# Performance work log

Hardware: AMD Instinct MI355X
Metric: run time of the kernel (lower is better)

Reference implementation:

```python
import jax, jax.numpy as jnp
import numpy as np

NUM_HEADS = 12
HEAD_DIM = 64
SCALE = HEAD_DIM ** -0.5


def setup_inputs() -> dict:
    key = jax.random.key(0)
    ks = jax.random.split(key, 5)
    B, N, C = 8, 1024, 768
    x = jax.random.normal(ks[0], (B, N, C), dtype=jnp.float32)
    qkv_w = jax.random.normal(ks[1], (3 * C, C), dtype=jnp.float32) * (C ** -0.5)
    qkv_b = jax.random.normal(ks[2], (3 * C,), dtype=jnp.float32) * 0.02
    proj_w = jax.random.normal(ks[3], (C, C), dtype=jnp.float32) * (C ** -0.5)
    proj_b = jax.random.normal(ks[4], (C,), dtype=jnp.float32) * 0.02
    return {"x": x, "qkv_w": qkv_w, "qkv_b": qkv_b, "proj_w": proj_w, "proj_b": proj_b}


def reference(x, qkv_w, qkv_b, proj_w, proj_b):
    B, N, C = x.shape
    H, D = NUM_HEADS, HEAD_DIM
    # qkv projection: (B,N,3C) -> (3,B,H,N,D)
    qkv = (x @ qkv_w.T + qkv_b).reshape(B, N, 3, H, D).transpose(2, 0, 3, 1, 4)
    q, k, v = qkv[0], qkv[1], qkv[2]
    q = q * SCALE
    # full N x N attention scores, softmax over keys
    attn = jax.nn.softmax(jnp.einsum("bhnd,bhmd->bhnm", q, k), axis=-1)
    # Libragrad: detach the softmax map before multiplying with V
    attn = jax.lax.stop_gradient(attn)
    out = jnp.einsum("bhnm,bhmd->bhnd", attn, v)  # (B,H,N,D)
    out = out.transpose(0, 2, 1, 3).reshape(B, N, C)
    return out @ proj_w.T + proj_b
```

## Files before the change

kernel.cpp:

```cpp
#include <hip/hip_runtime.h>

#define NH 12
#define HD 64
#define BB 8
#define SEQ 1024
#define CD 768

typedef __bf16 bf16x8 __attribute__((ext_vector_type(8)));
typedef float f32x4 __attribute__((ext_vector_type(4)));

__device__ __forceinline__ unsigned short f2bf(float f) {
    unsigned int u = __float_as_uint(f);
    u = (u + 0x7fffu + ((u >> 16) & 1u)) >> 16;
    return (unsigned short)u;
}

__device__ __forceinline__ void gld_lds16(const unsigned short* g, unsigned short* l) {
    __builtin_amdgcn_global_load_lds(
        (const __attribute__((address_space(1))) unsigned int*)g,
        (__attribute__((address_space(3))) unsigned int*)l, 16, 0, 0);
}

#define N4_X 1572864
#define N4_W1 442368
#define N4_W2 147456
__global__ void cast_all(const float* __restrict__ x, const float* __restrict__ w1,
                         const float* __restrict__ w2,
                         unsigned short* __restrict__ ox, unsigned short* __restrict__ ow1,
                         unsigned short* __restrict__ ow2) {
    int i = blockIdx.x * blockDim.x + threadIdx.x;
    const float4* src;
    ushort4* dst;
    if (i < N4_X) {
        src = (const float4*)x + i; dst = (ushort4*)ox + i;
    } else if (i < N4_X + N4_W1) {
        src = (const float4*)w1 + (i - N4_X); dst = (ushort4*)ow1 + (i - N4_X);
    } else if (i < N4_X + N4_W1 + N4_W2) {
        src = (const float4*)w2 + (i - N4_X - N4_W1); dst = (ushort4*)ow2 + (i - N4_X - N4_W1);
    } else return;
    float4 f = *src;
    ushort4 o;
    o.x = f2bf(f.x); o.y = f2bf(f.y); o.z = f2bf(f.z); o.w = f2bf(f.w);
    *dst = o;
}

template<int MODE>
__global__ __launch_bounds__(256)
void gemm_bt(const unsigned short* __restrict__ A, const unsigned short* __restrict__ W,
             const float* __restrict__ bias,
             unsigned short* __restrict__ qb, unsigned short* __restrict__ kb,
             unsigned short* __restrict__ vb, float* __restrict__ fout,
             int M, int N, int K) {
    __shared__ __attribute__((aligned(16))) unsigned short As[128 * 32];
    __shared__ __attribute__((aligned(16))) unsigned short Bs[128 * 32];

    const int t    = threadIdx.x;
    const int bn0  = blockIdx.x * 128;
    const int bm0  = blockIdx.y * 128;
    const int wave = t >> 6;
    const int lane = t & 63;
    const int wm   = (wave >> 1) * 64;
    const int wn   = (wave & 1) * 64;
    const int col  = lane & 15;
    const int quad = lane >> 4;

    const int srow = t >> 2;
    const int scol = (t & 3) * 8;

    f32x4 acc[4][4];
#pragma unroll
    for (int i = 0; i < 4; i++)
#pragma unroll
        for (int j = 0; j < 4; j++) acc[i][j] = (f32x4){0.f, 0.f, 0.f, 0.f};

    for (int k0 = 0; k0 < K; k0 += 32) {
        __syncthreads();
        gld_lds16(A + (size_t)(bm0 + srow) * K + k0 + scol,      As + srow * 32 + scol);
        gld_lds16(A + (size_t)(bm0 + 64 + srow) * K + k0 + scol, As + (64 + srow) * 32 + scol);
        gld_lds16(W + (size_t)(bn0 + srow) * K + k0 + scol,      Bs + srow * 32 + scol);
        gld_lds16(W + (size_t)(bn0 + 64 + srow) * K + k0 + scol, Bs + (64 + srow) * 32 + scol);
        __syncthreads();

        bf16x8 af[4], bf[4];
#pragma unroll
        for (int mi = 0; mi < 4; mi++)
            af[mi] = *(const bf16x8*)(As + (wm + mi * 16 + col) * 32 + quad * 8);
#pragma unroll
        for (int ni = 0; ni < 4; ni++)
            bf[ni] = *(const bf16x8*)(Bs + (wn + ni * 16 + col) * 32 + quad * 8);
#pragma unroll
        for (int mi = 0; mi < 4; mi++)
#pragma unroll
            for (int ni = 0; ni < 4; ni++)
                acc[mi][ni] = __builtin_amdgcn_mfma_f32_16x16x32_bf16(
                    af[mi], bf[ni], acc[mi][ni], 0, 0, 0);
    }

#pragma unroll
    for (int mi = 0; mi < 4; mi++) {
#pragma unroll
        for (int ni = 0; ni < 4; ni++) {
            const int n = bn0 + wn + ni * 16 + col;
            const float bv = bias[n];
#pragma unroll
            for (int r = 0; r < 4; r++) {
                const int m = bm0 + wm + mi * 16 + quad * 4 + r;
                float val = acc[mi][ni][r] + bv;
                if (MODE == 0) {
                    const int tq  = n / 768;
                    const int rem = n - tq * 768;
                    const int h   = rem >> 6;
                    const int d   = rem & 63;
                    const int b   = m >> 10;
                    const int nq  = m & 1023;
                    const size_t dst = ((size_t)(b * NH + h) * SEQ + nq) * HD + d;
                    if (tq == 0)      qb[dst] = f2bf(val * 0.125f);
                    else if (tq == 1) kb[dst] = f2bf(val);
                    else              vb[dst] = f2bf(val);
                } else {
                    fout[(size_t)m * N + n] = val;
                }
            }
        }
    }
}

__global__ __launch_bounds__(256)
void transpose_v(const unsigned short* __restrict__ v,
                 unsigned short* __restrict__ vt) {
    __shared__ unsigned short tile[64 * 72];
    const int bh = blockIdx.x;
    const int st = blockIdx.y;
    const int t  = threadIdx.x;
    const int sr = t >> 2;
    const int sc = (t & 3) * 16;

    const unsigned short* src = v + ((size_t)bh * SEQ + st * 64 + sr) * HD + sc;
    *(uint4*)(tile + sr * 72 + sc)     = *(const uint4*)src;
    *(uint4*)(tile + sr * 72 + sc + 8) = *(const uint4*)(src + 8);
    __syncthreads();

    union { unsigned short us[16]; uint4 u4[2]; } tmp;
#pragma unroll
    for (int i = 0; i < 16; i++) tmp.us[i] = tile[(sc + i) * 72 + sr];
    unsigned short* dst = vt + ((size_t)bh * HD + sr) * SEQ + st * 64 + sc;
    *(uint4*)dst       = tmp.u4[0];
    *(uint4*)(dst + 8) = tmp.u4[1];
}

__global__ __launch_bounds__(256, 3)
void attn_mfma(const unsigned short* __restrict__ qb,
               const unsigned short* __restrict__ kb,
               const unsigned short* __restrict__ vtb,
               unsigned short* __restrict__ ob) {
    __shared__ __attribute__((aligned(16))) unsigned short Ks[64 * 72];
    __shared__ __attribute__((aligned(16))) unsigned short VT[64 * 72];
    __shared__ __attribute__((aligned(16))) unsigned short Ps[128 * 76];

    const int t  = threadIdx.x;
    const int bh = blockIdx.x;
    const int qt = blockIdx.y;
    const size_t base  = (size_t)bh * SEQ * HD;
    const size_t vbase = (size_t)bh * HD * SEQ;

    const int sr = t >> 2;
    const int sc = (t & 3) * 16;

    const int wave = t >> 6;
    const int lane = t & 63;
    const int col  = lane & 15;
    const int quad = lane >> 4;

    bf16x8 aq[2][2];
#pragma unroll
    for (int u = 0; u < 2; u++) {
        const int q = qt * 128 + (2 * wave + u) * 16 + col;
        aq[u][0] = *(const bf16x8*)(qb + base + (size_t)q * HD + quad * 8);
        aq[u][1] = *(const bf16x8*)(qb + base + (size_t)q * HD + 32 + quad * 8);
    }

    float l_r[2][4];
#pragma unroll
    for (int u = 0; u < 2; u++)
#pragma unroll
        for (int r = 0; r < 4; r++) l_r[u][r] = 0.f;
    f32x4 accO[2][4];
#pragma unroll
    for (int u = 0; u < 2; u++)
#pragma unroll
        for (int di = 0; di < 4; di++) accO[u][di] = (f32x4){0.f, 0.f, 0.f, 0.f};

    const unsigned short* kp = kb + base + (size_t)sr * HD + sc;
    const unsigned short* vp = vtb + vbase + (size_t)sr * SEQ + sc;
    uint4 kr0 = *(const uint4*)kp,       kr1 = *(const uint4*)(kp + 8);
    uint4 vr0 = *(const uint4*)vp,       vr1 = *(const uint4*)(vp + 8);

    for (int kc = 0; kc < 16; kc++) {
        __syncthreads();
        *(uint4*)(Ks + sr * 72 + sc)     = kr0;
        *(uint4*)(Ks + sr * 72 + sc + 8) = kr1;
        *(uint4*)(VT + sr * 72 + sc)     = vr0;
        *(uint4*)(VT + sr * 72 + sc + 8) = vr1;
        __syncthreads();

        if (kc < 15) {
            const unsigned short* kn = kp + (size_t)(kc + 1) * 64 * HD;
            const unsigned short* vn = vp + (kc + 1) * 64;
            kr0 = *(const uint4*)kn; kr1 = *(const uint4*)(kn + 8);
            vr0 = *(const uint4*)vn; vr1 = *(const uint4*)(vn + 8);
        }

        f32x4 accS[2][4];
#pragma unroll
        for (int ni = 0; ni < 4; ni++) {
            bf16x8 bk0 = *(const bf16x8*)(Ks + (ni * 16 + col) * 72 + quad * 8);
            bf16x8 bk1 = *(const bf16x8*)(Ks + (ni * 16 + col) * 72 + 32 + quad * 8);
#pragma unroll
            for (int u = 0; u < 2; u++) {
                f32x4 z = (f32x4){0.f, 0.f, 0.f, 0.f};
                z = __builtin_amdgcn_mfma_f32_16x16x32_bf16(aq[u][0], bk0, z, 0, 0, 0);
                z = __builtin_amdgcn_mfma_f32_16x16x32_bf16(aq[u][1], bk1, z, 0, 0, 0);
                accS[u][ni] = z;
            }
        }

#pragma unroll
        for (int u = 0; u < 2; u++) {
            const int prow = (2 * wave + u) * 16;
#pragma unroll
            for (int r = 0; r < 4; r++) {
                float p0 = __expf(accS[u][0][r]);
                float p1 = __expf(accS[u][1][r]);
                float p2 = __expf(accS[u][2][r]);
                float p3 = __expf(accS[u][3][r]);
                l_r[u][r] += (p0 + p1) + (p2 + p3);
                const int row = (prow + quad * 4 + r) * 76;
                Ps[row + col]      = f2bf(p0);
                Ps[row + 16 + col] = f2bf(p1);
                Ps[row + 32 + col] = f2bf(p2);
                Ps[row + 48 + col] = f2bf(p3);
            }
        }

        bf16x8 ap[2][2];
#pragma unroll
        for (int u = 0; u < 2; u++) {
            const int prow = (2 * wave + u) * 16;
            ap[u][0] = *(const bf16x8*)(Ps + (prow + col) * 76 + quad * 8);
            ap[u][1] = *(const bf16x8*)(Ps + (prow + col) * 76 + 32 + quad * 8);
        }
#pragma unroll
        for (int di = 0; di < 4; di++) {
            bf16x8 bv0 = *(const bf16x8*)(VT + (di * 16 + col) * 72 + quad * 8);
            bf16x8 bv1 = *(const bf16x8*)(VT + (di * 16 + col) * 72 + 32 + quad * 8);
#pragma unroll
            for (int u = 0; u < 2; u++) {
                accO[u][di] = __builtin_amdgcn_mfma_f32_16x16x32_bf16(ap[u][0], bv0, accO[u][di], 0, 0, 0);
                accO[u][di] = __builtin_amdgcn_mfma_f32_16x16x32_bf16(ap[u][1], bv1, accO[u][di], 0, 0, 0);
            }
        }
    }

    const int b = bh / NH, h = bh - b * NH;
#pragma unroll
    for (int u = 0; u < 2; u++)
#pragma unroll
        for (int r = 0; r < 4; r++) {
            float s = l_r[u][r];
            s += __shfl_xor(s, 1);
            s += __shfl_xor(s, 2);
            s += __shfl_xor(s, 4);
            s += __shfl_xor(s, 8);
            const float inv = 1.f / s;
            const int q = qt * 128 + (2 * wave + u) * 16 + quad * 4 + r;
            const size_t rowbase = ((size_t)b * SEQ + q) * CD + h * 64;
#pragma unroll
            for (int di = 0; di < 4; di++)
                ob[rowbase + di * 16 + col] = f2bf(accO[u][di][r] * inv);
        }
}

extern "C" void kernel_launch(void* const* d_in, const int* in_sizes, int n_in,
                              void* d_out, int out_size, void* d_ws, size_t ws_size,
                              hipStream_t stream) {
    const float* x      = (const float*)d_in[0];
    const float* qkv_w  = (const float*)d_in[1];
    const float* qkv_b  = (const float*)d_in[2];
    const float* proj_w = (const float*)d_in[3];
    const float* proj_b = (const float*)d_in[4];
    float* out = (float*)d_out;

    char* ws = (char*)d_ws;
    unsigned short* x_bf     = (unsigned short*)ws;
    unsigned short* vt_bf    = x_bf;
    unsigned short* qkvw_bf  = (unsigned short*)(ws + 12582912);
    unsigned short* projw_bf = (unsigned short*)(ws + 12582912 + 3538944);
    unsigned short* q_bf     = (unsigned short*)(ws + 12582912 + 3538944 + 1179648);
    unsigned short* k_bf     = q_bf + 6291456;
    unsigned short* v_bf     = k_bf + 6291456;
    unsigned short* attn_bf  = v_bf;

    cast_all<<<8448, 256, 0, stream>>>(x, qkv_w, proj_w, x_bf, qkvw_bf, projw_bf);

    gemm_bt<0><<<dim3(18, 64), 256, 0, stream>>>(x_bf, qkvw_bf, qkv_b,
                                                 q_bf, k_bf, v_bf, nullptr,
                                                 8192, 2304, 768);

    transpose_v<<<dim3(96, 16), 256, 0, stream>>>(v_bf, vt_bf);

    attn_mfma<<<dim3(96, 8), 256, 0, stream>>>(q_bf, k_bf, vt_bf, attn_bf);

    gemm_bt<1><<<dim3(6, 64), 256, 0, stream>>>(attn_bf, projw_bf, proj_b,
                                                nullptr, nullptr, nullptr, out,
                                                8192, 768, 768);
}
```

Baseline: 212.2 us.

## Fuse V transpose into QKV GEMM epilogue with LDS-staged coalesced stores

The QKV GEMM epilogue now stages each 128x64 head tile through shared memory. It then writes Q and K rows with 16-byte vector stores, and writes V directly in transposed (d-major) layout. This removes the separate transpose_v kernel launch and its extra round trip of V through global memory. It also replaces the scattered 2-byte stores with coalesced writes. In exchange it adds barriers and a larger shared allocation in the GEMM, and the attention output buffer is moved to alias x_bf.

New measurement: 224.9 us. +6.0%, slower.

```diff
diff --git a/kernel.cpp b/kernel.cpp
--- a/kernel.cpp
+++ b/kernel.cpp
@@ -51,8 +51,9 @@
              unsigned short* __restrict__ qb, unsigned short* __restrict__ kb,
              unsigned short* __restrict__ vb, float* __restrict__ fout,
              int M, int N, int K) {
-    __shared__ __attribute__((aligned(16))) unsigned short As[128 * 32];
-    __shared__ __attribute__((aligned(16))) unsigned short Bs[128 * 32];
+    __shared__ __attribute__((aligned(16))) unsigned short smem[9216];
+    unsigned short* As = smem;
+    unsigned short* Bs = smem + 4096;
 
     const int t    = threadIdx.x;
     const int bn0  = blockIdx.x * 128;
@@ -96,56 +97,82 @@
                     af[mi], bf[ni], acc[mi][ni], 0, 0, 0);
     }
 
-#pragma unroll
-    for (int mi = 0; mi < 4; mi++) {
-#pragma unroll
-        for (int ni = 0; ni < 4; ni++) {
-            const int n = bn0 + wn + ni * 16 + col;
-            const float bv = bias[n];
-#pragma unroll
-            for (int r = 0; r < 4; r++) {
-                const int m = bm0 + wm + mi * 16 + quad * 4 + r;
-                float val = acc[mi][ni][r] + bv;
-                if (MODE == 0) {
-                    const int tq  = n / 768;
-                    const int rem = n - tq * 768;
-                    const int h   = rem >> 6;
-                    const int d   = rem & 63;
-                    const int b   = m >> 10;
-                    const int nq  = m & 1023;
-                    const size_t dst = ((size_t)(b * NH + h) * SEQ + nq) * HD + d;
-                    if (tq == 0)      qb[dst] = f2bf(val * 0.125f);
-                    else if (tq == 1) kb[dst] = f2bf(val);
-                    else              vb[dst] = f2bf(val);
-                } else {
-                    fout[(size_t)m * N + n] = val;
+    if (MODE == 1) {
+#pragma unroll
+        for (int mi = 0; mi < 4; mi++)
+#pragma unroll
+            for (int ni = 0; ni < 4; ni++) {
+                const int n = bn0 + wn + ni * 16 + col;
+                const float bv = bias[n];
+#pragma unroll
+                for (int r = 0; r < 4; r++) {
+                    const int m = bm0 + wm + mi * 16 + quad * 4 + r;
+                    fout[(size_t)m * N + n] = acc[mi][ni][r] + bv;
                 }
             }
-        }
-    }
-}
-
-__global__ __launch_bounds__(256)
-void transpose_v(const unsigned short* __restrict__ v,
-                 unsigned short* __restrict__ vt) {
-    __shared__ unsigned short tile[64 * 72];
-    const int bh = blockIdx.x;
-    const int st = blockIdx.y;
-    const int t  = threadIdx.x;
-    const int sr = t >> 2;
-    const int sc = (t & 3) * 16;
-
-    const unsigned short* src = v + ((size_t)bh * SEQ + st * 64 + sr) * HD + sc;
-    *(uint4*)(tile + sr * 72 + sc)     = *(const uint4*)src;
-    *(uint4*)(tile + sr * 72 + sc + 8) = *(const uint4*)(src + 8);
-    __syncthreads();
-
-    union { unsigned short us[16]; uint4 u4[2]; } tmp;
-#pragma unroll
-    for (int i = 0; i < 16; i++) tmp.us[i] = tile[(sc + i) * 72 + sr];
-    unsigned short* dst = vt + ((size_t)bh * HD + sr) * SEQ + st * 64 + sc;
-    *(uint4*)dst       = tmp.u4[0];
-    *(uint4*)(dst + 8) = tmp.u4[1];
+        return;
+    }
+
+    const int sel = bn0 / 768;
+    const int h0  = (bn0 - sel * 768) >> 6;
+    const int b   = bm0 >> 10;
+    const int nq0 = bm0 & 1023;
+
+    if (sel < 2) {
+        unsigned short* dstbuf = (sel == 0) ? qb : kb;
+        const float scale = (sel == 0) ? 0.125f : 1.0f;
+#pragma unroll
+        for (int hh = 0; hh < 2; hh++) {
+            __syncthreads();
+            if ((wave & 1) == hh) {
+#pragma unroll
+                for (int ni = 0; ni < 4; ni++) {
+                    const float bv = bias[bn0 + hh * 64 + ni * 16 + col];
+#pragma unroll
+                    for (int mi = 0; mi < 4; mi++)
+#pragma unroll
+                        for (int r = 0; r < 4; r++) {
+                            const int ml = wm + mi * 16 + quad * 4 + r;
+                            smem[ml * 72 + ni * 16 + col] =
+                                f2bf((acc[mi][ni][r] + bv) * scale);
+                        }
+                }
+            }
+            __syncthreads();
+            unsigned short* dst = dstbuf +
+                ((size_t)(b * NH + h0 + hh) * SEQ + nq0) * HD;
+            const int nq = t >> 1, c0 = (t & 1) * 32;
+            const uint4* s = (const uint4*)(smem + nq * 72 + c0);
+            uint4* g = (uint4*)(dst + nq * 64 + c0);
+            g[0] = s[0]; g[1] = s[1]; g[2] = s[2]; g[3] = s[3];
+        }
+    } else {
+#pragma unroll
+        for (int hh = 0; hh < 2; hh++) {
+            __syncthreads();
+            if ((wave & 1) == hh) {
+#pragma unroll
+                for (int ni = 0; ni < 4; ni++) {
+                    const float bv = bias[bn0 + hh * 64 + ni * 16 + col];
+#pragma unroll
+                    for (int mi = 0; mi < 4; mi++)
+#pragma unroll
+                        for (int r = 0; r < 4; r++) {
+                            const int ml = wm + mi * 16 + quad * 4 + r;
+                            smem[(ni * 16 + col) * 136 + ml] =
+                                f2bf(acc[mi][ni][r] + bv);
+                        }
+                }
+            }
+            __syncthreads();
+            const int d = t >> 2, c0 = (t & 3) * 32;
+            unsigned short* dst = vb +
+                ((size_t)(b * NH + h0 + hh) * HD + d) * SEQ + nq0 + c0;
+            const uint4* s = (const uint4*)(smem + d * 136 + c0);
+            uint4* g = (uint4*)dst;
+            g[0] = s[0]; g[1] = s[1]; g[2] = s[2]; g[3] = s[3];
+        }
+    }
 }
 
 __global__ __launch_bounds__(256, 3)
@@ -292,21 +319,18 @@
 
     char* ws = (char*)d_ws;
     unsigned short* x_bf     = (unsigned short*)ws;
-    unsigned short* vt_bf    = x_bf;
+    unsigned short* attn_bf  = x_bf;
     unsigned short* qkvw_bf  = (unsigned short*)(ws + 12582912);
     unsigned short* projw_bf = (unsigned short*)(ws + 12582912 + 3538944);
     unsigned short* q_bf     = (unsigned short*)(ws + 12582912 + 3538944 + 1179648);
     unsigned short* k_bf     = q_bf + 6291456;
-    unsigned short* v_bf     = k_bf + 6291456;
-    unsigned short* attn_bf  = v_bf;
+    unsigned short* vt_bf    = k_bf + 6291456;
 
     cast_all<<<8448, 256, 0, stream>>>(x, qkv_w, proj_w, x_bf, qkvw_bf, projw_bf);
 
     gemm_bt<0><<<dim3(18, 64), 256, 0, stream>>>(x_bf, qkvw_bf, qkv_b,
-                                                 q_bf, k_bf, v_bf, nullptr,
+                                                 q_bf, k_bf, vt_bf, nullptr,
                                                  8192, 2304, 768);
-
-    transpose_v<<<dim3(96, 16), 256, 0, stream>>>(v_bf, vt_bf);
 
     attn_mfma<<<dim3(96, 8), 256, 0, stream>>>(q_bf, k_bf, vt_bf, attn_bf);
 
```

## Load K/V MFMA fragments directly from global and swap GEMM grid order

Applied to the files above, without the earlier changes.

The attention kernel no longer stages K and V^T tiles in shared memory. Each lane loads its MFMA B-operand fragments straight from global memory into registers, with K prefetched one chunk ahead, which removes two block barriers per key chunk and the LDS round trip. Each wave now fetches the full K/V tile itself instead of sharing one copy across the four waves, so global/L2 traffic and register pressure go up. Separately, the GEMM grids are transposed so that consecutive blocks walk the M dimension, which changes the order in which tiles are scheduled and how much of the data is reused from cache.

Result: slower. 255.7 us (+20.5%).

```diff
diff --git a/kernel.cpp b/kernel.cpp
--- a/kernel.cpp
+++ b/kernel.cpp
@@ -55,8 +55,8 @@
     __shared__ __attribute__((aligned(16))) unsigned short Bs[128 * 32];
 
     const int t    = threadIdx.x;
-    const int bn0  = blockIdx.x * 128;
-    const int bm0  = blockIdx.y * 128;
+    const int bm0  = blockIdx.x * 128;
+    const int bn0  = blockIdx.y * 128;
     const int wave = t >> 6;
     const int lane = t & 63;
     const int wm   = (wave >> 1) * 64;
@@ -153,8 +153,6 @@
                const unsigned short* __restrict__ kb,
                const unsigned short* __restrict__ vtb,
                unsigned short* __restrict__ ob) {
-    __shared__ __attribute__((aligned(16))) unsigned short Ks[64 * 72];
-    __shared__ __attribute__((aligned(16))) unsigned short VT[64 * 72];
     __shared__ __attribute__((aligned(16))) unsigned short Ps[128 * 76];
 
     const int t  = threadIdx.x;
@@ -163,9 +161,6 @@
     const size_t base  = (size_t)bh * SEQ * HD;
     const size_t vbase = (size_t)bh * HD * SEQ;
 
-    const int sr = t >> 2;
-    const int sc = (t & 3) * 16;
-
     const int wave = t >> 6;
     const int lane = t & 63;
     const int col  = lane & 15;
@@ -179,6 +174,9 @@
         aq[u][1] = *(const bf16x8*)(qb + base + (size_t)q * HD + 32 + quad * 8);
     }
 
+    const unsigned short* kf = kb  + base  + (size_t)col * HD  + quad * 8;
+    const unsigned short* vf = vtb + vbase + (size_t)col * SEQ + quad * 8;
+
     float l_r[2][4];
 #pragma unroll
     for (int u = 0; u < 2; u++)
@@ -190,37 +188,39 @@
 #pragma unroll
         for (int di = 0; di < 4; di++) accO[u][di] = (f32x4){0.f, 0.f, 0.f, 0.f};
 
-    const unsigned short* kp = kb + base + (size_t)sr * HD + sc;
-    const unsigned short* vp = vtb + vbase + (size_t)sr * SEQ + sc;
-    uint4 kr0 = *(const uint4*)kp,       kr1 = *(const uint4*)(kp + 8);
-    uint4 vr0 = *(const uint4*)vp,       vr1 = *(const uint4*)(vp + 8);
+    bf16x8 bk[4][2];
+#pragma unroll
+    for (int ni = 0; ni < 4; ni++) {
+        bk[ni][0] = *(const bf16x8*)(kf + (size_t)ni * 16 * HD);
+        bk[ni][1] = *(const bf16x8*)(kf + (size_t)ni * 16 * HD + 32);
+    }
 
     for (int kc = 0; kc < 16; kc++) {
-        __syncthreads();
-        *(uint4*)(Ks + sr * 72 + sc)     = kr0;
-        *(uint4*)(Ks + sr * 72 + sc + 8) = kr1;
-        *(uint4*)(VT + sr * 72 + sc)     = vr0;
-        *(uint4*)(VT + sr * 72 + sc + 8) = vr1;
-        __syncthreads();
-
-        if (kc < 15) {
-            const unsigned short* kn = kp + (size_t)(kc + 1) * 64 * HD;
-            const unsigned short* vn = vp + (kc + 1) * 64;
-            kr0 = *(const uint4*)kn; kr1 = *(const uint4*)(kn + 8);
-            vr0 = *(const uint4*)vn; vr1 = *(const uint4*)(vn + 8);
+        bf16x8 bv[4][2];
+#pragma unroll
+        for (int di = 0; di < 4; di++) {
+            const unsigned short* vp = vf + (size_t)di * 16 * SEQ + kc * 64;
+            bv[di][0] = *(const bf16x8*)vp;
+            bv[di][1] = *(const bf16x8*)(vp + 32);
         }
 
         f32x4 accS[2][4];
 #pragma unroll
-        for (int ni = 0; ni < 4; ni++) {
-            bf16x8 bk0 = *(const bf16x8*)(Ks + (ni * 16 + col) * 72 + quad * 8);
-            bf16x8 bk1 = *(const bf16x8*)(Ks + (ni * 16 + col) * 72 + 32 + quad * 8);
+        for (int ni = 0; ni < 4; ni++)
 #pragma unroll
             for (int u = 0; u < 2; u++) {
                 f32x4 z = (f32x4){0.f, 0.f, 0.f, 0.f};
-                z = __builtin_amdgcn_mfma_f32_16x16x32_bf16(aq[u][0], bk0, z, 0, 0, 0);
-                z = __builtin_amdgcn_mfma_f32_16x16x32_bf16(aq[u][1], bk1, z, 0, 0, 0);
+                z = __builtin_amdgcn_mfma_f32_16x16x32_bf16(aq[u][0], bk[ni][0], z, 0, 0, 0);
+                z = __builtin_amdgcn_mfma_f32_16x16x32_bf16(aq[u][1], bk[ni][1], z, 0, 0, 0);
                 accS[u][ni] = z;
+            }
+
+        if (kc < 15) {
+            const unsigned short* kn = kf + (size_t)(kc + 1) * 64 * HD;
+#pragma unroll
+            for (int ni = 0; ni < 4; ni++) {
+                bk[ni][0] = *(const bf16x8*)(kn + (size_t)ni * 16 * HD);
+                bk[ni][1] = *(const bf16x8*)(kn + (size_t)ni * 16 * HD + 32);
             }
         }
 
@@ -250,15 +250,12 @@
             ap[u][1] = *(const bf16x8*)(Ps + (prow + col) * 76 + 32 + quad * 8);
         }
 #pragma unroll
-        for (int di = 0; di < 4; di++) {
-            bf16x8 bv0 = *(const bf16x8*)(VT + (di * 16 + col) * 72 + quad * 8);
-            bf16x8 bv1 = *(const bf16x8*)(VT + (di * 16 + col) * 72 + 32 + quad * 8);
+        for (int di = 0; di < 4; di++)
 #pragma unroll
             for (int u = 0; u < 2; u++) {
-                accO[u][di] = __builtin_amdgcn_mfma_f32_16x16x32_bf16(ap[u][0], bv0, accO[u][di], 0, 0, 0);
-                accO[u][di] = __builtin_amdgcn_mfma_f32_16x16x32_bf16(ap[u][1], bv1, accO[u][di], 0, 0, 0);
-            }
-        }
+                accO[u][di] = __builtin_amdgcn_mfma_f32_16x16x32_bf16(ap[u][0], bv[di][0], accO[u][di], 0, 0, 0);
+                accO[u][di] = __builtin_amdgcn_mfma_f32_16x16x32_bf16(ap[u][1], bv[di][1], accO[u][di], 0, 0, 0);
+            }
     }
 
     const int b = bh / NH, h = bh - b * NH;
@@ -302,7 +299,7 @@
 
     cast_all<<<8448, 256, 0, stream>>>(x, qkv_w, proj_w, x_bf, qkvw_bf, projw_bf);
 
-    gemm_bt<0><<<dim3(18, 64), 256, 0, stream>>>(x_bf, qkvw_bf, qkv_b,
+    gemm_bt<0><<<dim3(64, 18), 256, 0, stream>>>(x_bf, qkvw_bf, qkv_b,
                                                  q_bf, k_bf, v_bf, nullptr,
                                                  8192, 2304, 768);
 
@@ -310,7 +307,7 @@
 
     attn_mfma<<<dim3(96, 8), 256, 0, stream>>>(q_bf, k_bf, vt_bf, attn_bf);
 
-    gemm_bt<1><<<dim3(6, 64), 256, 0, stream>>>(attn_bf, projw_bf, proj_b,
+    gemm_bt<1><<<dim3(64, 6), 256, 0, stream>>>(attn_bf, projw_bf, proj_b,
                                                 nullptr, nullptr, nullptr, out,
                                                 8192, 768, 768);
 }
```
